# Optimization experiments

Measured on AMD Instinct MI355X. Metric: run time of the kernel, lower is better.

The kernel has to match this reference:

```python
import jax, jax.numpy as jnp
import numpy as np

N_NODES = 50000


def gcn_conv(x, W, b, src, dst, n_nodes):
    # PyG GCNConv: add self-loops, symmetric normalization, linear, scatter-add.
    loop = jnp.arange(n_nodes, dtype=src.dtype)
    s = jnp.concatenate([src, loop])  # [E+N]
    d = jnp.concatenate([dst, loop])
    deg = jax.ops.segment_sum(jnp.ones_like(d, dtype=x.dtype), d, num_segments=n_nodes)
    dinv = jnp.where(deg > 0, deg ** -0.5, 0.0)
    norm = dinv[s] * dinv[d]  # [E+N]
    h = x @ W  # [N, F_out] transform first (cheaper than per-edge)
    msg = h[s] * norm[:, None]  # gather + scale
    out = jax.ops.segment_sum(msg, d, num_segments=n_nodes)  # scatter-add
    return out + b


def setup_inputs() -> dict:
    key = jax.random.key(0)
    k1, k2, k3, k4, k5 = jax.random.split(key, 5)
    n_in, n_hid, n_out = 128, 128, 64
    x = jax.random.normal(k1, (N_NODES, n_in), dtype=jnp.float32)
    edge_index = jax.random.randint(k2, (2, 800000), 0, N_NODES, dtype=jnp.int64)
    edge_label_index = jax.random.randint(k3, (2, 200000), 0, N_NODES, dtype=jnp.int64)
    # Glorot-style init for GCN weights, zero bias (PyG default)
    W1 = jax.random.normal(k4, (n_in, n_hid), dtype=jnp.float32) * (1.0 / np.sqrt(n_in))
    W2 = jax.random.normal(k5, (n_hid, n_out), dtype=jnp.float32) * (1.0 / np.sqrt(n_hid))
    b1 = jnp.zeros((n_hid,), dtype=jnp.float32)
    b2 = jnp.zeros((n_out,), dtype=jnp.float32)
    return {"x": x, "edge_index": edge_index, "edge_label_index": edge_label_index,
            "W1": W1, "b1": b1, "W2": W2, "b2": b2}


def reference(x, edge_index, edge_label_index, W1, b1, W2, b2):
    src, dst = edge_index[0], edge_index[1]
    h = jax.nn.relu(gcn_conv(x, W1, b1, src, dst, N_NODES))
    z = gcn_conv(h, W2, b2, src, dst, N_NODES)
    # decode: per-edge dot product of endpoint embeddings
    logits = jnp.sum(z[edge_label_index[0]] * z[edge_label_index[1]], axis=-1)
    return logits
```

## Files before the change

### kernel.cpp

```cpp
#include <hip/hip_runtime.h>

#define N_NODES 50000
#define NB ((N_NODES + 255) / 256)

using half8 = __attribute__((ext_vector_type(8))) _Float16;
using half4 = __attribute__((ext_vector_type(4))) _Float16;
using f32x4 = __attribute__((ext_vector_type(4))) float;


#define OFF_ROWPTR 50048
#define OFF_BSUM   100096
#define OFF_BOFF   100352
#define OFF_CNT    100608
#define OFF_ESRC   150656
#define OFF_EPOS   950656
#define OFF_W1T    1750656
#define OFF_W2T    1758848
#define OFF_H1B    1762944
#define OFF_OUT1   4962944
#define OFF_Z      11362944

__device__ __forceinline__ ushort f2bf(float f) {
  uint u = __float_as_uint(f);
  u += 0x7fffu + ((u >> 16) & 1u);
  return (ushort)(u >> 16);
}
__device__ __forceinline__ uint pack2(float a, float b) {
  return (uint)f2bf(a) | ((uint)f2bf(b) << 16);
}
__device__ __forceinline__ float blo(uint u) { return __uint_as_float(u << 16); }
__device__ __forceinline__ float bhi(uint u) { return __uint_as_float(u & 0xffff0000u); }

__global__ __launch_bounds__(256) void k_zero_prep(int* __restrict__ cnt,
                                                   const float* __restrict__ W1,
                                                   const float* __restrict__ W2,
                                                   _Float16* __restrict__ W1t,
                                                   _Float16* __restrict__ W2t) {
  int bid = blockIdx.x;
  if (bid < NB) {
    int i = bid * 256 + threadIdx.x;
    if (i < N_NODES) cnt[i] = 0;
    return;
  }
  int i = (bid - NB) * 256 + threadIdx.x;
  if (i < 16384) {
    int c = i >> 7, k = i & 127;
    W1t[c * 128 + (k ^ ((c & 7) << 3))] = (_Float16)W1[k * 128 + c];
  } else if (i < 24576) {
    int j = i - 16384;
    int c = j >> 7, k = j & 127;
    W2t[c * 128 + (k ^ ((c & 7) << 3))] = (_Float16)W2[k * 64 + c];
  }
}

__global__ __launch_bounds__(256) void k_hist(const int* __restrict__ dst, int E,
                                              int* __restrict__ cnt,
                                              int* __restrict__ epos) {
  int i = blockIdx.x * 256 + threadIdx.x;
  if (i < E) epos[i] = atomicAdd(&cnt[dst[i]], 1);
}

__global__ __launch_bounds__(256) void k_scan1(const int* __restrict__ cnt,
                                               int* __restrict__ rowptr,
                                               int* __restrict__ bsum) {
  __shared__ int tmp[256];
  int i = blockIdx.x * 256 + threadIdx.x;
  int v = (i < N_NODES) ? cnt[i] : 0;
  tmp[threadIdx.x] = v;
  __syncthreads();
  for (int off = 1; off < 256; off <<= 1) {
    int t = (threadIdx.x >= off) ? tmp[threadIdx.x - off] : 0;
    __syncthreads();
    tmp[threadIdx.x] += t;
    __syncthreads();
  }
  if (i < N_NODES) rowptr[i] = tmp[threadIdx.x] - v;
  if (threadIdx.x == 255) bsum[blockIdx.x] = tmp[255];
}

__global__ __launch_bounds__(256) void k_scan2(const int* __restrict__ bsum,
                                               int* __restrict__ boff) {
  __shared__ int tmp[256];
  int v = (threadIdx.x < NB) ? bsum[threadIdx.x] : 0;
  tmp[threadIdx.x] = v;
  __syncthreads();
  for (int off = 1; off < 256; off <<= 1) {
    int t = (threadIdx.x >= off) ? tmp[threadIdx.x - off] : 0;
    __syncthreads();
    tmp[threadIdx.x] += t;
    __syncthreads();
  }
  if (threadIdx.x < NB) boff[threadIdx.x] = tmp[threadIdx.x] - v;
}

__global__ __launch_bounds__(256) void k_scan3(int* __restrict__ rowptr,
                                               const int* __restrict__ cnt,
                                               float* __restrict__ dinv,
                                               const int* __restrict__ boff, int E) {
  int i = blockIdx.x * 256 + threadIdx.x;
  if (i < N_NODES) {
    rowptr[i] += boff[blockIdx.x];
    dinv[i] = rsqrtf(1.0f + (float)cnt[i]);
  }
  if (i == 0) rowptr[N_NODES] = E;
}

__global__ __launch_bounds__(256) void k_fill(const int* __restrict__ src,
                                              const int* __restrict__ dst,
                                              const int* __restrict__ epos, int E,
                                              const int* __restrict__ rowptr,
                                              int* __restrict__ esrc) {
  int e = blockIdx.x * 256 + threadIdx.x;
  if (e < E) esrc[rowptr[dst[e]] + epos[e]] = src[e];
}

__global__ __launch_bounds__(256) void k_gemm1(const float* __restrict__ x,
                                               const _Float16* __restrict__ W1t,
                                               const float* __restrict__ dinv,
                                               ushort* __restrict__ h1b) {
  __shared__ _Float16 Wl[128 * 128];
  __shared__ _Float16 xs[64 * 128];
  const int tid = threadIdx.x;
  const int lane = tid & 63;
  const int wv = tid >> 6;
  const int n0 = blockIdx.x * 64;

  for (int i = tid; i < 128 * 128 / 8; i += 256)
    *(float4*)&Wl[i * 8] = *(const float4*)&W1t[i * 8];
  for (int i = tid; i < 64 * 32; i += 256) {
    int nn = i >> 5, k4 = (i & 31) * 4;
    int gr = min(n0 + nn, N_NODES - 1);
    float4 v = *(const float4*)&x[(size_t)gr * 128 + k4];
    half4 hv;
    hv[0] = (_Float16)v.x; hv[1] = (_Float16)v.y;
    hv[2] = (_Float16)v.z; hv[3] = (_Float16)v.w;
    *(half4*)&xs[nn * 128 + (k4 ^ ((nn & 7) << 3))] = hv;
  }
  __syncthreads();

  f32x4 acc[8];
#pragma unroll
  for (int c = 0; c < 8; ++c) acc[c] = (f32x4){0.f, 0.f, 0.f, 0.f};

  const int m15 = lane & 15;
  const int kc = lane >> 4;
  const int xrow = wv * 16 + m15;

#pragma unroll
  for (int kt = 0; kt < 4; ++kt) {
    int e0 = kt * 32 + kc * 8;
    half8 bfrag = *(half8*)&xs[xrow * 128 + (e0 ^ ((xrow & 7) << 3))];
#pragma unroll
    for (int ct = 0; ct < 8; ++ct) {
      int wrow = ct * 16 + m15;
      half8 afrag = *(half8*)&Wl[wrow * 128 + (e0 ^ ((wrow & 7) << 3))];
      acc[ct] = __builtin_amdgcn_mfma_f32_16x16x32_f16(afrag, bfrag, acc[ct], 0, 0, 0);
    }
  }

  int n = n0 + wv * 16 + m15;
  if (n < N_NODES) {
    float dl = dinv[n];
#pragma unroll
    for (int ct = 0; ct < 8; ++ct) {
      int c = ct * 16 + kc * 4;
      uint2 p;
      p.x = pack2(acc[ct][0] * dl, acc[ct][1] * dl);
      p.y = pack2(acc[ct][2] * dl, acc[ct][3] * dl);
      *(uint2*)&h1b[(size_t)n * 128 + c] = p;
    }
  }
}

__global__ __launch_bounds__(256) void k_pull1(const int* __restrict__ rowptr,
                                               const int* __restrict__ esrc,
                                               const float* __restrict__ dinv,
                                               const uint* __restrict__ h1b,
                                               const float* __restrict__ b1,
                                               float* __restrict__ out1) {
  int n = (blockIdx.x * 256 + threadIdx.x) >> 6;
  int lane = threadIdx.x & 63;
  if (n >= N_NODES) return;
  int b = rowptr[n], e = rowptr[n + 1];
  int deg = e - b;

  uint u = h1b[(size_t)n * 64 + lane];
  float a0 = blo(u), a1 = bhi(u);

  int sidx = (lane < deg) ? esrc[b + lane] : 0;
  int kmax = deg < 64 ? deg : 64;
  int k = 0;
  for (; k + 15 < kmax; k += 16) {
    uint uu[16];
#pragma unroll
    for (int q = 0; q < 16; ++q) {
      int s = __shfl(sidx, k + q, 64);
      uu[q] = h1b[(size_t)s * 64 + lane];
    }
#pragma unroll
    for (int q = 0; q < 16; ++q) { a0 += blo(uu[q]); a1 += bhi(uu[q]); }
  }
  for (; k + 7 < kmax; k += 8) {
    uint uu[8];
#pragma unroll
    for (int q = 0; q < 8; ++q) {
      int s = __shfl(sidx, k + q, 64);
      uu[q] = h1b[(size_t)s * 64 + lane];
    }
#pragma unroll
    for (int q = 0; q < 8; ++q) { a0 += blo(uu[q]); a1 += bhi(uu[q]); }
  }
  for (; k < kmax; ++k) {
    int s = __shfl(sidx, k, 64);
    uint uu = h1b[(size_t)s * 64 + lane];
    a0 += blo(uu);
    a1 += bhi(uu);
  }
  for (int j = b + 64; j < e; ++j) {
    uint uu = h1b[(size_t)esrc[j] * 64 + lane];
    a0 += blo(uu);
    a1 += bhi(uu);
  }

  float dd = dinv[n];
  float2 bb = ((const float2*)b1)[lane];
  float2 o;
  o.x = fmaf(dd, a0, bb.x);
  o.y = fmaf(dd, a1, bb.y);
  ((float2*)out1)[(size_t)n * 64 + lane] = o;
}

__global__ __launch_bounds__(256) void k_gemm2(const float* __restrict__ out1,
                                               const _Float16* __restrict__ W2t,
                                               const float* __restrict__ dinv,
                                               ushort* __restrict__ h2b) {
  __shared__ _Float16 Wl[64 * 128];
  __shared__ _Float16 xs[64 * 128];
  const int tid = threadIdx.x;
  const int lane = tid & 63;
  const int wv = tid >> 6;
  const int n0 = blockIdx.x * 64;

  for (int i = tid; i < 64 * 128 / 8; i += 256)
    *(float4*)&Wl[i * 8] = *(const float4*)&W2t[i * 8];
  for (int i = tid; i < 64 * 32; i += 256) {
    int nn = i >> 5, k4 = (i & 31) * 4;
    int gr = min(n0 + nn, N_NODES - 1);
    float4 v = *(const float4*)&out1[(size_t)gr * 128 + k4];
    half4 hv;
    hv[0] = (_Float16)fmaxf(v.x, 0.f); hv[1] = (_Float16)fmaxf(v.y, 0.f);
    hv[2] = (_Float16)fmaxf(v.z, 0.f); hv[3] = (_Float16)fmaxf(v.w, 0.f);
    *(half4*)&xs[nn * 128 + (k4 ^ ((nn & 7) << 3))] = hv;
  }
  __syncthreads();

  f32x4 acc[4];
#pragma unroll
  for (int c = 0; c < 4; ++c) acc[c] = (f32x4){0.f, 0.f, 0.f, 0.f};

  const int m15 = lane & 15;
  const int kc = lane >> 4;
  const int xrow = wv * 16 + m15;

#pragma unroll
  for (int kt = 0; kt < 4; ++kt) {
    int e0 = kt * 32 + kc * 8;
    half8 bfrag = *(half8*)&xs[xrow * 128 + (e0 ^ ((xrow & 7) << 3))];
#pragma unroll
    for (int ct = 0; ct < 4; ++ct) {
      int wrow = ct * 16 + m15;
      half8 afrag = *(half8*)&Wl[wrow * 128 + (e0 ^ ((wrow & 7) << 3))];
      acc[ct] = __builtin_amdgcn_mfma_f32_16x16x32_f16(afrag, bfrag, acc[ct], 0, 0, 0);
    }
  }

  int n = n0 + wv * 16 + m15;
  if (n < N_NODES) {
    float dl = dinv[n];
#pragma unroll
    for (int ct = 0; ct < 4; ++ct) {
      int c = ct * 16 + kc * 4;
      uint2 p;
      p.x = pack2(acc[ct][0] * dl, acc[ct][1] * dl);
      p.y = pack2(acc[ct][2] * dl, acc[ct][3] * dl);
      *(uint2*)&h2b[(size_t)n * 64 + c] = p;
    }
  }
}

__global__ __launch_bounds__(256) void k_pull2(const int* __restrict__ rowptr,
                                               const int* __restrict__ esrc,
                                               const float* __restrict__ dinv,
                                               const ushort* __restrict__ h2b,
                                               const float* __restrict__ b2,
                                               _Float16* __restrict__ z) {
  int n = (blockIdx.x * 256 + threadIdx.x) >> 6;
  int lane = threadIdx.x & 63;
  if (n >= N_NODES) return;
  int b = rowptr[n], e = rowptr[n + 1];
  int deg = e - b;

  float a = __uint_as_float((uint)h2b[(size_t)n * 64 + lane] << 16);

  int sidx = (lane < deg) ? esrc[b + lane] : 0;
  int kmax = deg < 64 ? deg : 64;
  int k = 0;
  for (; k + 15 < kmax; k += 16) {
    ushort vv[16];
#pragma unroll
    for (int q = 0; q < 16; ++q) {
      int s = __shfl(sidx, k + q, 64);
      vv[q] = h2b[(size_t)s * 64 + lane];
    }
#pragma unroll
    for (int q = 0; q < 16; ++q) a += __uint_as_float((uint)vv[q] << 16);
  }
  for (; k + 7 < kmax; k += 8) {
    ushort vv[8];
#pragma unroll
    for (int q = 0; q < 8; ++q) {
      int s = __shfl(sidx, k + q, 64);
      vv[q] = h2b[(size_t)s * 64 + lane];
    }
#pragma unroll
    for (int q = 0; q < 8; ++q) a += __uint_as_float((uint)vv[q] << 16);
  }
  for (; k < kmax; ++k) {
    int s = __shfl(sidx, k, 64);
    a += __uint_as_float((uint)h2b[(size_t)s * 64 + lane] << 16);
  }
  for (int j = b + 64; j < e; ++j)
    a += __uint_as_float((uint)h2b[(size_t)esrc[j] * 64 + lane] << 16);

  z[(size_t)n * 64 + lane] = (_Float16)fmaf(dinv[n], a, b2[lane]);
}

__global__ __launch_bounds__(256) void k_decode(const int* __restrict__ ia,
                                                const int* __restrict__ ib,
                                                const _Float16* __restrict__ z,
                                                float* __restrict__ out, int M) {
  const int sub = threadIdx.x & 7;
  int e = (blockIdx.x * 256 + threadIdx.x) >> 3;
  if (e >= M) return;
  int a = ia[e], b = ib[e];
  half8 va = ((const half8*)z)[(size_t)a * 8 + sub];
  half8 vb = ((const half8*)z)[(size_t)b * 8 + sub];
  float v = 0.f;
#pragma unroll
  for (int i = 0; i < 8; ++i) v += (float)va[i] * (float)vb[i];
  v += __shfl_xor(v, 4, 64);
  v += __shfl_xor(v, 2, 64);
  v += __shfl_xor(v, 1, 64);
  if (sub == 0) out[e] = v;
}

extern "C" void kernel_launch(void* const* d_in, const int* in_sizes, int n_in,
                              void* d_out, int out_size, void* d_ws, size_t ws_size,
                              hipStream_t stream) {
  const float* x   = (const float*)d_in[0];
  const int*   ei  = (const int*)d_in[1];
  const int*   eli = (const int*)d_in[2];
  const float* W1  = (const float*)d_in[3];
  const float* b1  = (const float*)d_in[4];
  const float* W2  = (const float*)d_in[5];
  const float* b2  = (const float*)d_in[6];
  float* outp = (float*)d_out;

  const int E = in_sizes[1] / 2;
  const int M = in_sizes[2] / 2;
  const int* src = ei;
  const int* dst = ei + E;
  const int* la  = eli;
  const int* lb  = eli + M;

  float* ws     = (float*)d_ws;
  float* dinv   = ws;
  int*   rowptr = (int*)(ws + OFF_ROWPTR);
  int*   bsum   = (int*)(ws + OFF_BSUM);
  int*   boff   = (int*)(ws + OFF_BOFF);
  int*   cnt    = (int*)(ws + OFF_CNT);
  int*   esrc   = (int*)(ws + OFF_ESRC);
  int*   epos   = (int*)(ws + OFF_EPOS);
  _Float16* W1t = (_Float16*)(ws + OFF_W1T);
  _Float16* W2t = (_Float16*)(ws + OFF_W2T);
  ushort* h1b   = (ushort*)(ws + OFF_H1B);
  ushort* h2b   = (ushort*)(ws + OFF_H1B);
  float* out1   = ws + OFF_OUT1;
  _Float16* z   = (_Float16*)(ws + OFF_Z);

  k_zero_prep<<<NB + 96, 256, 0, stream>>>(cnt, W1, W2, W1t, W2t);
  k_hist <<<(E + 255) / 256, 256, 0, stream>>>(dst, E, cnt, epos);
  k_scan1<<<NB, 256, 0, stream>>>(cnt, rowptr, bsum);
  k_scan2<<<1, 256, 0, stream>>>(bsum, boff);
  k_scan3<<<NB, 256, 0, stream>>>(rowptr, cnt, dinv, boff, E);
  k_fill <<<(E + 255) / 256, 256, 0, stream>>>(src, dst, epos, E, rowptr, esrc);

  k_gemm1<<<(N_NODES + 63) / 64, 256, 0, stream>>>(x, W1t, dinv, h1b);
  k_pull1<<<12500, 256, 0, stream>>>(rowptr, esrc, dinv, (const uint*)h1b, b1, out1);

  k_gemm2<<<(N_NODES + 63) / 64, 256, 0, stream>>>(out1, W2t, dinv, h2b);
  k_pull2<<<12500, 256, 0, stream>>>(rowptr, esrc, dinv, h2b, b2, z);

  k_decode<<<6250, 256, 0, stream>>>(la, lb, z, outp, M);
}
```

Baseline: 226.5 us.

## Merge scan kernels into decoupled look-back scan and store layer-1 output as fp16

Replaces the three-kernel prefix sum (block scan, block-sum scan, fixup) with one single-pass scan that uses decoupled look-back descriptors, removing two launches and a round trip through global memory. The layer-1 aggregation now writes its output as packed fp16 instead of fp32. The second GEMM then loads half8 vectors and applies ReLU in fp16, which halves the intermediate traffic. The look-back spin-waits on earlier blocks and relies on forward-progress ordering, and fp16 storage can overflow or lose precision for large values.

```diff
diff --git a/kernel.cpp b/kernel.cpp
--- a/kernel.cpp
+++ b/kernel.cpp
@@ -9,8 +9,7 @@
 
 
 #define OFF_ROWPTR 50048
-#define OFF_BSUM   100096
-#define OFF_BOFF   100352
+#define OFF_DESC   100096
 #define OFF_CNT    100608
 #define OFF_ESRC   150656
 #define OFF_EPOS   950656
@@ -18,7 +17,7 @@
 #define OFF_W2T    1758848
 #define OFF_H1B    1762944
 #define OFF_OUT1   4962944
-#define OFF_Z      11362944
+#define OFF_Z      8162944
 
 __device__ __forceinline__ ushort f2bf(float f) {
   uint u = __float_as_uint(f);
@@ -28,10 +27,16 @@
 __device__ __forceinline__ uint pack2(float a, float b) {
   return (uint)f2bf(a) | ((uint)f2bf(b) << 16);
 }
+__device__ __forceinline__ uint pack2h(float a, float b) {
+  ushort ua = __builtin_bit_cast(ushort, (_Float16)a);
+  ushort ub = __builtin_bit_cast(ushort, (_Float16)b);
+  return (uint)ua | ((uint)ub << 16);
+}
 __device__ __forceinline__ float blo(uint u) { return __uint_as_float(u << 16); }
 __device__ __forceinline__ float bhi(uint u) { return __uint_as_float(u & 0xffff0000u); }
 
 __global__ __launch_bounds__(256) void k_zero_prep(int* __restrict__ cnt,
+                                                   uint* __restrict__ desc,
                                                    const float* __restrict__ W1,
                                                    const float* __restrict__ W2,
                                                    _Float16* __restrict__ W1t,
@@ -40,6 +45,7 @@
   if (bid < NB) {
     int i = bid * 256 + threadIdx.x;
     if (i < N_NODES) cnt[i] = 0;
+    if (bid == 0 && threadIdx.x < NB) desc[threadIdx.x] = 0;
     return;
   }
   int i = (bid - NB) * 256 + threadIdx.x;
@@ -60,11 +66,14 @@
   if (i < E) epos[i] = atomicAdd(&cnt[dst[i]], 1);
 }
 
-__global__ __launch_bounds__(256) void k_scan1(const int* __restrict__ cnt,
-                                               int* __restrict__ rowptr,
-                                               int* __restrict__ bsum) {
+__global__ __launch_bounds__(256) void k_scanlb(const int* __restrict__ cnt,
+                                                int* __restrict__ rowptr,
+                                                float* __restrict__ dinv,
+                                                uint* __restrict__ desc, int E) {
   __shared__ int tmp[256];
-  int i = blockIdx.x * 256 + threadIdx.x;
+  __shared__ int s_prefix;
+  const int b = blockIdx.x;
+  const int i = b * 256 + threadIdx.x;
   int v = (i < N_NODES) ? cnt[i] : 0;
   tmp[threadIdx.x] = v;
   __syncthreads();
@@ -74,35 +83,36 @@
     tmp[threadIdx.x] += t;
     __syncthreads();
   }
-  if (i < N_NODES) rowptr[i] = tmp[threadIdx.x] - v;
-  if (threadIdx.x == 255) bsum[blockIdx.x] = tmp[255];
-}
-
-__global__ __launch_bounds__(256) void k_scan2(const int* __restrict__ bsum,
-                                               int* __restrict__ boff) {
-  __shared__ int tmp[256];
-  int v = (threadIdx.x < NB) ? bsum[threadIdx.x] : 0;
-  tmp[threadIdx.x] = v;
+  int incl = tmp[threadIdx.x];
+  int total = tmp[255];
+
+  if (threadIdx.x == 0) {
+    if (b == 0) {
+      atomicExch(&desc[0], (2u << 30) | (uint)total);
+      s_prefix = 0;
+    } else {
+      atomicExch(&desc[b], (1u << 30) | (uint)total);
+      int run = 0;
+      int j = b - 1;
+      while (true) {
+        uint w = atomicAdd(&desc[j], 0u);
+        uint st = w >> 30;
+        if (st == 0u) continue;
+        run += (int)(w & 0x3FFFFFFFu);
+        if (st == 2u) break;
+        --j;
+      }
+      atomicExch(&desc[b], (2u << 30) | (uint)(run + total));
+      s_prefix = run;
+    }
+  }
   __syncthreads();
-  for (int off = 1; off < 256; off <<= 1) {
-    int t = (threadIdx.x >= off) ? tmp[threadIdx.x - off] : 0;
-    __syncthreads();
-    tmp[threadIdx.x] += t;
-    __syncthreads();
-  }
-  if (threadIdx.x < NB) boff[threadIdx.x] = tmp[threadIdx.x] - v;
-}
-
-__global__ __launch_bounds__(256) void k_scan3(int* __restrict__ rowptr,
-                                               const int* __restrict__ cnt,
-                                               float* __restrict__ dinv,
-                                               const int* __restrict__ boff, int E) {
-  int i = blockIdx.x * 256 + threadIdx.x;
+  int run = s_prefix;
   if (i < N_NODES) {
-    rowptr[i] += boff[blockIdx.x];
-    dinv[i] = rsqrtf(1.0f + (float)cnt[i]);
-  }
-  if (i == 0) rowptr[N_NODES] = E;
+    rowptr[i] = run + incl - v;
+    dinv[i] = rsqrtf(1.0f + (float)v);
+  }
+  if (b == NB - 1 && threadIdx.x == 0) rowptr[N_NODES] = E;
 }
 
 __global__ __launch_bounds__(256) void k_fill(const int* __restrict__ src,
@@ -177,7 +187,7 @@
                                                const float* __restrict__ dinv,
                                                const uint* __restrict__ h1b,
                                                const float* __restrict__ b1,
-                                               float* __restrict__ out1) {
+                                               uint* __restrict__ out1h) {
   int n = (blockIdx.x * 256 + threadIdx.x) >> 6;
   int lane = threadIdx.x & 63;
   if (n >= N_NODES) return;
@@ -224,13 +234,10 @@
 
   float dd = dinv[n];
   float2 bb = ((const float2*)b1)[lane];
-  float2 o;
-  o.x = fmaf(dd, a0, bb.x);
-  o.y = fmaf(dd, a1, bb.y);
-  ((float2*)out1)[(size_t)n * 64 + lane] = o;
-}
-
-__global__ __launch_bounds__(256) void k_gemm2(const float* __restrict__ out1,
+  out1h[(size_t)n * 64 + lane] = pack2h(fmaf(dd, a0, bb.x), fmaf(dd, a1, bb.y));
+}
+
+__global__ __launch_bounds__(256) void k_gemm2(const _Float16* __restrict__ out1h,
                                                const _Float16* __restrict__ W2t,
                                                const float* __restrict__ dinv,
                                                ushort* __restrict__ h2b) {
@@ -243,14 +250,13 @@
 
   for (int i = tid; i < 64 * 128 / 8; i += 256)
     *(float4*)&Wl[i * 8] = *(const float4*)&W2t[i * 8];
-  for (int i = tid; i < 64 * 32; i += 256) {
-    int nn = i >> 5, k4 = (i & 31) * 4;
+  for (int i = tid; i < 64 * 16; i += 256) {
+    int nn = i >> 4, k8 = (i & 15) * 8;
     int gr = min(n0 + nn, N_NODES - 1);
-    float4 v = *(const float4*)&out1[(size_t)gr * 128 + k4];
-    half4 hv;
-    hv[0] = (_Float16)fmaxf(v.x, 0.f); hv[1] = (_Float16)fmaxf(v.y, 0.f);
-    hv[2] = (_Float16)fmaxf(v.z, 0.f); hv[3] = (_Float16)fmaxf(v.w, 0.f);
-    *(half4*)&xs[nn * 128 + (k4 ^ ((nn & 7) << 3))] = hv;
+    half8 v = *(const half8*)&out1h[(size_t)gr * 128 + k8];
+#pragma unroll
+    for (int q = 0; q < 8; ++q) v[q] = v[q] > (_Float16)0.f ? v[q] : (_Float16)0.f;
+    *(half8*)&xs[nn * 128 + (k8 ^ ((nn & 7) << 3))] = v;
   }
   __syncthreads();
 
@@ -373,32 +379,30 @@
   const int* la  = eli;
   const int* lb  = eli + M;
 
-  float* ws     = (float*)d_ws;
-  float* dinv   = ws;
-  int*   rowptr = (int*)(ws + OFF_ROWPTR);
-  int*   bsum   = (int*)(ws + OFF_BSUM);
-  int*   boff   = (int*)(ws + OFF_BOFF);
-  int*   cnt    = (int*)(ws + OFF_CNT);
-  int*   esrc   = (int*)(ws + OFF_ESRC);
-  int*   epos   = (int*)(ws + OFF_EPOS);
-  _Float16* W1t = (_Float16*)(ws + OFF_W1T);
-  _Float16* W2t = (_Float16*)(ws + OFF_W2T);
-  ushort* h1b   = (ushort*)(ws + OFF_H1B);
-  ushort* h2b   = (ushort*)(ws + OFF_H1B);
-  float* out1   = ws + OFF_OUT1;
-  _Float16* z   = (_Float16*)(ws + OFF_Z);
-
-  k_zero_prep<<<NB + 96, 256, 0, stream>>>(cnt, W1, W2, W1t, W2t);
-  k_hist <<<(E + 255) / 256, 256, 0, stream>>>(dst, E, cnt, epos);
-  k_scan1<<<NB, 256, 0, stream>>>(cnt, rowptr, bsum);
-  k_scan2<<<1, 256, 0, stream>>>(bsum, boff);
-  k_scan3<<<NB, 256, 0, stream>>>(rowptr, cnt, dinv, boff, E);
-  k_fill <<<(E + 255) / 256, 256, 0, stream>>>(src, dst, epos, E, rowptr, esrc);
+  float* ws      = (float*)d_ws;
+  float* dinv    = ws;
+  int*   rowptr  = (int*)(ws + OFF_ROWPTR);
+  uint*  desc    = (uint*)(ws + OFF_DESC);
+  int*   cnt     = (int*)(ws + OFF_CNT);
+  int*   esrc    = (int*)(ws + OFF_ESRC);
+  int*   epos    = (int*)(ws + OFF_EPOS);
+  _Float16* W1t  = (_Float16*)(ws + OFF_W1T);
+  _Float16* W2t  = (_Float16*)(ws + OFF_W2T);
+  ushort* h1b    = (ushort*)(ws + OFF_H1B);
+  ushort* h2b    = (ushort*)(ws + OFF_H1B);
+  _Float16* out1h = (_Float16*)(ws + OFF_OUT1);
+  _Float16* z    = (_Float16*)(ws + OFF_Z);
+
+  k_zero_prep<<<NB + 96, 256, 0, stream>>>(cnt, desc, W1, W2, W1t, W2t);
+  k_hist  <<<(E + 255) / 256, 256, 0, stream>>>(dst, E, cnt, epos);
+  k_scanlb<<<NB, 256, 0, stream>>>(cnt, rowptr, dinv, desc, E);
+  k_fill  <<<(E + 255) / 256, 256, 0, stream>>>(src, dst, epos, E, rowptr, esrc);
 
   k_gemm1<<<(N_NODES + 63) / 64, 256, 0, stream>>>(x, W1t, dinv, h1b);
-  k_pull1<<<12500, 256, 0, stream>>>(rowptr, esrc, dinv, (const uint*)h1b, b1, out1);
-
-  k_gemm2<<<(N_NODES + 63) / 64, 256, 0, stream>>>(out1, W2t, dinv, h2b);
+  k_pull1<<<12500, 256, 0, stream>>>(rowptr, esrc, dinv, (const uint*)h1b, b1,
+                                     (uint*)out1h);
+
+  k_gemm2<<<(N_NODES + 63) / 64, 256, 0, stream>>>(out1h, W2t, dinv, h2b);
   k_pull2<<<12500, 256, 0, stream>>>(rowptr, esrc, dinv, h2b, b2, z);
 
   k_decode<<<6250, 256, 0, stream>>>(la, lb, z, outp, M);
```

Result: slower. 233.3 us (+3.0%).
